# Performance work log

Measured on AMD Instinct MI355X. Metric: run time of the kernel, lower is better.

## Reference

```python
import jax, jax.numpy as jnp
import numpy as np

B, L, C_S, H = 1, 512, 384, 12
D = C_S // H  # head_dim = 32


def setup_inputs() -> dict:
    key = jax.random.key(0)
    ks = jax.random.split(key, 12)
    sc = 1.0 / np.sqrt(C_S)
    inp = {
        "s": jax.random.normal(ks[0], (B, L, C_S), dtype=jnp.float32),
        "z": jax.random.normal(ks[1], (B, L, L, C_S), dtype=jnp.float32),
        "mask": jax.random.randint(ks[2], (B, L), 0, 2, dtype=jnp.int32),
        # learned params
        "Wq": jax.random.normal(ks[3], (C_S, H * D), dtype=jnp.float32) * sc,
        "bq": jnp.zeros((H * D,), dtype=jnp.float32),
        "Wkv": jax.random.normal(ks[4], (C_S, 2 * H * D), dtype=jnp.float32) * sc,
        "bkv": jnp.zeros((2 * H * D,), dtype=jnp.float32),
        "Wb": jax.random.normal(ks[5], (C_S, H), dtype=jnp.float32) * sc,
        "bb": jnp.zeros((H,), dtype=jnp.float32),
        "Wg": jax.random.normal(ks[6], (C_S, H), dtype=jnp.float32) * sc,
        "bg": jnp.zeros((H,), dtype=jnp.float32),
        "Wout": jax.random.normal(ks[7], (H * D, C_S), dtype=jnp.float32) * sc,
        "bout": jnp.zeros((C_S,), dtype=jnp.float32),
    }
    return inp


def reference(s, z, Wq, bq, Wkv, bkv, Wb, bb, Wg, bg, Wout, bout, mask):
    b, l, c = s.shape
    q = (s @ Wq + bq).reshape(b, l, H, D)                 # (B,L,h,d)
    kv = (s @ Wkv + bkv).reshape(b, l, 2, H, D)
    k, v = kv[:, :, 0], kv[:, :, 1]                       # (B,L,h,d)
    logits = jnp.einsum('blhd,bmhd->bhlm', q, k) * (D ** -0.5)
    bias = jnp.transpose(z @ Wb + bb, (0, 3, 1, 2))       # (B,h,L,L)
    logits = logits + bias
    gate = jax.nn.sigmoid(jnp.transpose(z @ Wg + bg, (0, 3, 1, 2)))
    maskf = mask.astype(logits.dtype)
    mask2d = maskf[:, :, None] * maskf[:, None, :]        # (B,L,L)
    logits = jnp.where(mask2d[:, None] < 0.5, jnp.asarray(-1e9, logits.dtype), logits)
    attn = jax.nn.softmax(logits, axis=-1) * gate         # (B,h,L,L)
    o = jnp.einsum('bhlm,bmhd->blhd', attn, v).reshape(b, l, H * D)
    return o @ Wout + bout
```

## Files before the change

kernel.cpp:

```cpp
#include <hip/hip_runtime.h>
#include <math.h>


typedef float vf4 __attribute__((ext_vector_type(4)));
typedef __attribute__((address_space(3))) void       lds_vp;
typedef __attribute__((address_space(1))) const void gm_vp;

__global__ __launch_bounds__(256) void sgemm_bias(const float* __restrict__ A, int lda,
                                                  const float* __restrict__ B, int ldb,
                                                  const float* __restrict__ bias,
                                                  float* __restrict__ C, int ldc, int K)
{
    __shared__ float As[32 * 36];
    __shared__ float Bs[32 * 68];

    const int t  = threadIdx.x;
    const int m0 = blockIdx.y * 32;
    const int n0 = blockIdx.x * 64;
    const int tx = t & 15;
    const int ty = t >> 4;

    float acc[2][4];
    #pragma unroll
    for (int i = 0; i < 2; ++i)
        #pragma unroll
        for (int j = 0; j < 4; ++j) acc[i][j] = 0.f;

    for (int kc = 0; kc < K; kc += 32) {
        __syncthreads();
        {
            int r = t >> 3, c = (t & 7) * 4;
            float4 av = *(const float4*)&A[(size_t)(m0 + r) * lda + kc + c];
            As[(c + 0) * 36 + r] = av.x;
            As[(c + 1) * 36 + r] = av.y;
            As[(c + 2) * 36 + r] = av.z;
            As[(c + 3) * 36 + r] = av.w;
        }
        #pragma unroll
        for (int i = 0; i < 2; ++i) {
            int slot = i * 256 + t;
            int r = slot >> 4, c = (slot & 15) * 4;
            *(float4*)&Bs[r * 68 + c] = *(const float4*)&B[(size_t)(kc + r) * ldb + n0 + c];
        }
        __syncthreads();
        #pragma unroll 8
        for (int k = 0; k < 32; ++k) {
            float2 a = *(const float2*)&As[k * 36 + ty * 2];
            float4 b = *(const float4*)&Bs[k * 68 + tx * 4];
            acc[0][0] = fmaf(a.x, b.x, acc[0][0]);
            acc[0][1] = fmaf(a.x, b.y, acc[0][1]);
            acc[0][2] = fmaf(a.x, b.z, acc[0][2]);
            acc[0][3] = fmaf(a.x, b.w, acc[0][3]);
            acc[1][0] = fmaf(a.y, b.x, acc[1][0]);
            acc[1][1] = fmaf(a.y, b.y, acc[1][1]);
            acc[1][2] = fmaf(a.y, b.z, acc[1][2]);
            acc[1][3] = fmaf(a.y, b.w, acc[1][3]);
        }
    }

    float4 bv = *(const float4*)&bias[n0 + tx * 4];
    #pragma unroll
    for (int im = 0; im < 2; ++im) {
        float4 r;
        r.x = acc[im][0] + bv.x;
        r.y = acc[im][1] + bv.y;
        r.z = acc[im][2] + bv.z;
        r.w = acc[im][3] + bv.w;
        *(float4*)&C[(size_t)(m0 + ty * 2 + im) * ldc + n0 + tx * 4] = r;
    }
}

__global__ __launch_bounds__(256) void wcat_kernel(const float* __restrict__ Wb,
                                                   const float* __restrict__ Wg,
                                                   float* __restrict__ wcat)
{
    int idx = blockIdx.x * 256 + threadIdx.x;
    if (idx < 24 * 384) {
        int hh = idx / 384, k = idx % 384;
        wcat[idx] = (hh < 12) ? Wb[k * 12 + hh] : Wg[k * 12 + (hh - 12)];
    }
}

__global__ __launch_bounds__(256) void biasgate_kernel(const float* __restrict__ z,
                                                       const float* __restrict__ wcat,
                                                       const float* __restrict__ bb,
                                                       const float* __restrict__ bg,
                                                       float* __restrict__ bias_out,
                                                       float* __restrict__ gate_out)
{
    __shared__ float zt[2][256 * 32];

    const int t  = threadIdx.x;
    const size_t p0 = (size_t)blockIdx.x * 256;
    const size_t p  = p0 + t;

    const int wv   = t >> 6;
    const int lane = t & 63;
    const int lrow = lane >> 3;
    const int lcol = (lane & 7) * 4;

    float acc[24];
    #pragma unroll
    for (int h = 0; h < 24; ++h) acc[h] = 0.f;

    #pragma unroll
    for (int i = 0; i < 8; ++i) {
        const int row = wv * 64 + i * 8 + lrow;
        __builtin_amdgcn_global_load_lds(
            (gm_vp*)(z + (p0 + row) * 384 + lcol),
            (lds_vp*)(&zt[0][row * 32 + lcol]), 16, 0, 0);
    }
    __syncthreads();

    #pragma unroll 1
    for (int c = 0; c < 12; ++c) {
        const int cur = c & 1;
        if (c < 11) {
            const int nk = (c + 1) * 32;
            #pragma unroll
            for (int i = 0; i < 8; ++i) {
                const int row = wv * 64 + i * 8 + lrow;
                __builtin_amdgcn_global_load_lds(
                    (gm_vp*)(z + (p0 + row) * 384 + nk + lcol),
                    (lds_vp*)(&zt[cur ^ 1][row * 32 + lcol]), 16, 0, 0);
            }
        }
        const int kc = c * 32;
        #pragma unroll
        for (int k4 = 0; k4 < 8; ++k4) {
            const vf4 zv = *(const vf4*)&zt[cur][t * 32 + k4 * 4];
            const float* wp = wcat + kc + k4 * 4;
            #pragma unroll
            for (int hh = 0; hh < 24; ++hh) {
                float4 w = *(const float4*)&wp[hh * 384];
                acc[hh] = fmaf(zv.x, w.x,
                          fmaf(zv.y, w.y,
                          fmaf(zv.z, w.z,
                          fmaf(zv.w, w.w, acc[hh]))));
            }
        }
        __syncthreads();
    }

    #pragma unroll
    for (int hh = 0; hh < 12; ++hh)
        bias_out[(size_t)hh * 262144 + p] = acc[hh] + bb[hh];
    #pragma unroll
    for (int hh = 0; hh < 12; ++hh) {
        float x = acc[12 + hh] + bg[hh];
        gate_out[(size_t)hh * 262144 + p] = 1.f / (1.f + expf(-x));
    }
}

__global__ __launch_bounds__(256) void attn_kernel(const float* __restrict__ q_ws,
                                                   const float* __restrict__ kv_ws,
                                                   const float* __restrict__ bias_ws,
                                                   const float* __restrict__ gate_ws,
                                                   const int* __restrict__ mask,
                                                   float* __restrict__ o_ws)
{
    __shared__ float ql[16 * 36];
    __shared__ float kl[128 * 36];
    __shared__ float att[16 * 516];
    __shared__ int   mint[16];

    const int t  = threadIdx.x;
    const int h  = blockIdx.y;
    const int i0 = blockIdx.x * 16;

    for (int idx = t; idx < 512; idx += 256) {
        int ii = idx >> 5, d = idx & 31;
        ql[ii * 36 + d] = q_ws[(size_t)(i0 + ii) * 384 + h * 32 + d];
    }
    if (t < 16) mint[t] = mask[i0 + t];

    const float inv = 0.17677669529663687f;
    const int jl = t & 127;
    const int ip = t >> 7;

    for (int jc = 0; jc < 4; ++jc) {
        const int j0 = jc * 128;
        __syncthreads();
        for (int idx = t; idx < 4096; idx += 256) {
            int jj = idx >> 5, d = idx & 31;
            kl[jj * 36 + d] = kv_ws[(size_t)(j0 + jj) * 768 + h * 32 + d];
        }
        __syncthreads();
        float4 kr[8];
        #pragma unroll
        for (int x = 0; x < 8; ++x) kr[x] = *(const float4*)&kl[jl * 36 + x * 4];
        const int mj = mask[j0 + jl];
        #pragma unroll
        for (int rr = 0; rr < 8; ++rr) {
            int ii = ip + rr * 2;
            float dot = 0.f;
            #pragma unroll
            for (int x = 0; x < 8; ++x) {
                float4 qv = *(const float4*)&ql[ii * 36 + x * 4];
                dot = fmaf(kr[x].x, qv.x, dot);
                dot = fmaf(kr[x].y, qv.y, dot);
                dot = fmaf(kr[x].z, qv.z, dot);
                dot = fmaf(kr[x].w, qv.w, dot);
            }
            float bv = bias_ws[((size_t)h << 18) + (size_t)(i0 + ii) * 512 + j0 + jl];
            float lg = fmaf(dot, inv, bv);
            att[ii * 516 + j0 + jl] = (mint[ii] != 0 && mj != 0) ? lg : -1e9f;
        }
    }
    __syncthreads();

    {
        const int rr = t >> 4, g = t & 15;
        const int base = rr * 516 + g;
        float mx = -3.0e38f;
        #pragma unroll
        for (int n = 0; n < 32; ++n) mx = fmaxf(mx, att[base + n * 16]);
        #pragma unroll
        for (int off = 8; off >= 1; off >>= 1) mx = fmaxf(mx, __shfl_xor(mx, off));
        float sum = 0.f;
        #pragma unroll
        for (int n = 0; n < 32; ++n) {
            float e = expf(att[base + n * 16] - mx);
            att[base + n * 16] = e;
            sum += e;
        }
        #pragma unroll
        for (int off = 8; off >= 1; off >>= 1) sum += __shfl_xor(sum, off);
        float isum = 1.f / sum;
        const size_t gbase = ((size_t)h << 18) + (size_t)(i0 + rr) * 512 + g;
        #pragma unroll
        for (int n = 0; n < 32; ++n) {
            float gt = gate_ws[gbase + n * 16];
            att[base + n * 16] *= isum * gt;
        }
    }
    __syncthreads();

    {
        const int d = t & 31, grp = t >> 5;
        const float* vp = kv_ws + 384 + h * 32 + d;
        float a0 = 0.f, a1 = 0.f;
        #pragma unroll 8
        for (int j = 0; j < 512; ++j) {
            float vv = vp[(size_t)j * 768];
            a0 = fmaf(att[grp * 516 + j], vv, a0);
            a1 = fmaf(att[(grp + 8) * 516 + j], vv, a1);
        }
        o_ws[(size_t)(i0 + grp) * 384 + h * 32 + d]     = a0;
        o_ws[(size_t)(i0 + grp + 8) * 384 + h * 32 + d] = a1;
    }
}

extern "C" void kernel_launch(void* const* d_in, const int* in_sizes, int n_in,
                              void* d_out, int out_size, void* d_ws, size_t ws_size,
                              hipStream_t stream)
{
    const float* s    = (const float*)d_in[0];
    const float* z    = (const float*)d_in[1];
    const int*   mask = (const int*)  d_in[2];
    const float* Wq   = (const float*)d_in[3];
    const float* bq   = (const float*)d_in[4];
    const float* Wkv  = (const float*)d_in[5];
    const float* bkv  = (const float*)d_in[6];
    const float* Wb   = (const float*)d_in[7];
    const float* bb   = (const float*)d_in[8];
    const float* Wg   = (const float*)d_in[9];
    const float* bg   = (const float*)d_in[10];
    const float* Wout = (const float*)d_in[11];
    const float* bout = (const float*)d_in[12];
    float* out = (float*)d_out;

    float* ws      = (float*)d_ws;
    float* q_ws    = ws;
    float* kv_ws   = q_ws + 512 * 384;
    float* o_ws    = kv_ws + 512 * 768;
    float* bias_ws = o_ws + 512 * 384;
    float* gate_ws = bias_ws + 12 * 512 * 512;
    float* wcat_ws = gate_ws + 12 * 512 * 512;

    wcat_kernel<<<36, 256, 0, stream>>>(Wb, Wg, wcat_ws);
    sgemm_bias<<<dim3(384 / 64, 512 / 32), 256, 0, stream>>>(s, 384, Wq, 384, bq, q_ws, 384, 384);
    sgemm_bias<<<dim3(768 / 64, 512 / 32), 256, 0, stream>>>(s, 384, Wkv, 768, bkv, kv_ws, 768, 384);
    biasgate_kernel<<<1024, 256, 0, stream>>>(z, wcat_ws, bb, bg, bias_ws, gate_ws);
    attn_kernel<<<dim3(512 / 16, 12), 256, 0, stream>>>(q_ws, kv_ws, bias_ws, gate_ws, mask, o_ws);
    sgemm_bias<<<dim3(384 / 64, 512 / 32), 256, 0, stream>>>(o_ws, 384, Wout, 384, bout, out, 384, 384);
}
```

Before: 769.2 us.

## Split biasgate K-dimension across thread halves with swizzled LDS and reduction

```diff
diff --git a/kernel.cpp b/kernel.cpp
--- a/kernel.cpp
+++ b/kernel.cpp
@@ -88,27 +88,31 @@
                                                        float* __restrict__ bias_out,
                                                        float* __restrict__ gate_out)
 {
-    __shared__ float zt[2][256 * 32];
-
-    const int t  = threadIdx.x;
-    const size_t p0 = (size_t)blockIdx.x * 256;
-    const size_t p  = p0 + t;
+    __shared__ float zt[2][128 * 32];
+
+    const int t    = threadIdx.x;
+    const size_t p0 = (size_t)blockIdx.x * 128;
 
     const int wv   = t >> 6;
     const int lane = t & 63;
     const int lrow = lane >> 3;
-    const int lcol = (lane & 7) * 4;
+    const int lcol = lane & 7;
+    const int scg  = lcol ^ lrow;
+
+    const int s = t >> 7;
+    const int p = t & 127;
+    const int psw = p & 7;
 
     float acc[24];
     #pragma unroll
     for (int h = 0; h < 24; ++h) acc[h] = 0.f;
 
     #pragma unroll
-    for (int i = 0; i < 8; ++i) {
-        const int row = wv * 64 + i * 8 + lrow;
+    for (int i = 0; i < 4; ++i) {
+        const int row = wv * 32 + i * 8 + lrow;
         __builtin_amdgcn_global_load_lds(
-            (gm_vp*)(z + (p0 + row) * 384 + lcol),
-            (lds_vp*)(&zt[0][row * 32 + lcol]), 16, 0, 0);
+            (gm_vp*)(z + (p0 + row) * 384 + scg * 4),
+            (lds_vp*)(&zt[0][row * 32 + lcol * 4]), 16, 0, 0);
     }
     __syncthreads();
 
@@ -118,18 +122,19 @@
         if (c < 11) {
             const int nk = (c + 1) * 32;
             #pragma unroll
-            for (int i = 0; i < 8; ++i) {
-                const int row = wv * 64 + i * 8 + lrow;
+            for (int i = 0; i < 4; ++i) {
+                const int row = wv * 32 + i * 8 + lrow;
                 __builtin_amdgcn_global_load_lds(
-                    (gm_vp*)(z + (p0 + row) * 384 + nk + lcol),
-                    (lds_vp*)(&zt[cur ^ 1][row * 32 + lcol]), 16, 0, 0);
+                    (gm_vp*)(z + (p0 + row) * 384 + nk + scg * 4),
+                    (lds_vp*)(&zt[cur ^ 1][row * 32 + lcol * 4]), 16, 0, 0);
             }
         }
         const int kc = c * 32;
         #pragma unroll
-        for (int k4 = 0; k4 < 8; ++k4) {
-            const vf4 zv = *(const vf4*)&zt[cur][t * 32 + k4 * 4];
-            const float* wp = wcat + kc + k4 * 4;
+        for (int q = 0; q < 4; ++q) {
+            const int c4 = s * 4 + q;
+            const vf4 zv = *(const vf4*)&zt[cur][p * 32 + (c4 ^ psw) * 4];
+            const float* wp = wcat + kc + c4 * 4;
             #pragma unroll
             for (int hh = 0; hh < 24; ++hh) {
                 float4 w = *(const float4*)&wp[hh * 384];
@@ -142,13 +147,22 @@
         __syncthreads();
     }
 
-    #pragma unroll
-    for (int hh = 0; hh < 12; ++hh)
-        bias_out[(size_t)hh * 262144 + p] = acc[hh] + bb[hh];
-    #pragma unroll
-    for (int hh = 0; hh < 12; ++hh) {
-        float x = acc[12 + hh] + bg[hh];
-        gate_out[(size_t)hh * 262144 + p] = 1.f / (1.f + expf(-x));
+    float* red = &zt[0][0];
+    if (s == 1) {
+        #pragma unroll
+        for (int hh = 0; hh < 24; ++hh) red[hh * 128 + p] = acc[hh];
+    }
+    __syncthreads();
+    if (s == 0) {
+        const size_t P = p0 + p;
+        #pragma unroll
+        for (int hh = 0; hh < 12; ++hh)
+            bias_out[(size_t)hh * 262144 + P] = acc[hh] + red[hh * 128 + p] + bb[hh];
+        #pragma unroll
+        for (int hh = 0; hh < 12; ++hh) {
+            float x = acc[12 + hh] + red[(12 + hh) * 128 + p] + bg[hh];
+            gate_out[(size_t)hh * 262144 + P] = 1.f / (1.f + expf(-x));
+        }
     }
 }
 
@@ -281,7 +295,7 @@
     wcat_kernel<<<36, 256, 0, stream>>>(Wb, Wg, wcat_ws);
     sgemm_bias<<<dim3(384 / 64, 512 / 32), 256, 0, stream>>>(s, 384, Wq, 384, bq, q_ws, 384, 384);
     sgemm_bias<<<dim3(768 / 64, 512 / 32), 256, 0, stream>>>(s, 384, Wkv, 768, bkv, kv_ws, 768, 384);
-    biasgate_kernel<<<1024, 256, 0, stream>>>(z, wcat_ws, bb, bg, bias_ws, gate_ws);
+    biasgate_kernel<<<2048, 256, 0, stream>>>(z, wcat_ws, bb, bg, bias_ws, gate_ws);
     attn_kernel<<<dim3(512 / 16, 12), 256, 0, stream>>>(q_ws, kv_ws, bias_ws, gate_ws, mask, o_ws);
     sgemm_bias<<<dim3(384 / 64, 512 / 32), 256, 0, stream>>>(o_ws, 384, Wout, 384, bout, out, 384, 384);
 }
```

Result: slower. 910.8 us (+18.4%).
